# Kernel tuning notes

Measured on AMD Instinct MI355X. Metric: run time of the kernel, lower is better.

The kernel has to match this reference:

```python
import jax, jax.numpy as jnp
from jax import lax
import numpy as np

BN_EPS = 1e-5
LN_EPS = 1e-5


def _ln(x, g, b):
    m = x.mean(-1, keepdims=True)
    v = ((x - m) ** 2).mean(-1, keepdims=True)
    return (x - m) / jnp.sqrt(v + LN_EPS) * g + b


def _bn(x, g, b):
    # eval-mode BatchNorm2d with running_mean=0, running_var=1
    s = g / np.float32(np.sqrt(1.0 + BN_EPS))
    return x * s[None, :, None, None] + b[None, :, None, None]


def _conv(x, w, b, pad=0):
    y = lax.conv_general_dilated(x, w, (1, 1), [(pad, pad), (pad, pad)],
                                 dimension_numbers=('NCHW', 'OIHW', 'NCHW'))
    return y + b[None, :, None, None]


def _t2p(t, H, W):  # token2patch: [B,N,C] -> [B,C,H,W]
    B, N, C = t.shape
    return t.transpose(0, 2, 1).reshape(B, C, H, W)


def _p2t(x):  # patch2token: [B,C,H,W] -> [B,H*W,C]
    B, C, H, W = x.shape
    return x.reshape(B, C, H * W).transpose(0, 2, 1)


def _sgn(x, cw, cr_w, cr_b, ci_w, ci_b, g1, b1, g2, b2):
    # SpectralGatingNetwork. x: [B,C,H,W]; torch permute(0,3,2,1) -> [B,W,H,C]
    xp = x.transpose(0, 3, 2, 1)
    f = jnp.fft.rfft2(xp, axes=(1, 2), norm='ortho')  # [B,W,H//2+1,C]
    fr = jax.nn.relu(_bn(_conv(f.real.transpose(0, 3, 1, 2), cr_w, cr_b), g1, b1))
    fi = jax.nn.relu(_bn(_conv(f.imag.transpose(0, 3, 1, 2), ci_w, ci_b), g2, b2))
    fc = (fr + 1j * fi).transpose(0, 2, 3, 1) * (cw[..., 0] + 1j * cw[..., 1])
    out = jnp.fft.irfft2(fc, s=(xp.shape[1], xp.shape[2]), axes=(1, 2), norm='ortho')
    return out.transpose(0, 3, 2, 1)


def _forward(p):
    x = p['x']
    B, N, D = x.shape
    # ---- Attention_Module (self.sum) ----
    y = jax.nn.relu(x @ p['am_lin_w'] + p['am_lin_b'])  # [B,N,8]
    H, dh = 8, 1  # Attention(8, num_heads=8) -> head_dim 1, scale 1
    qkv = (y @ p['am_qkv_w'] + p['am_qkv_b']).reshape(B, N, 3, H, dh).transpose(2, 0, 3, 1, 4)
    q, k, v = qkv[0], qkv[1], qkv[2]
    attn = jax.nn.softmax(jnp.einsum('bhnd,bhmd->bhnm', q, k) * (dh ** -0.5), axis=-1)
    av = jnp.einsum('bhnm,bhmd->bhnd', attn, v).transpose(0, 2, 1, 3).reshape(B, N, 8)
    av = av @ p['am_proj_w'] + p['am_proj_b']
    x0 = _ln(x + (y + av) @ p['am_end_w'] + p['am_end_b'], p['am_ln_g'], p['am_ln_b'])
    # ---- mlp2(norm2(x0)), timm Mlp hidden=dim, exact GELU ----
    h = _ln(x0, p['ln2_g'], p['ln2_b'])
    x0 = jax.nn.gelu(h @ p['mlp_fc1_w'] + p['mlp_fc1_b'], approximate=False) @ p['mlp_fc2_w'] + p['mlp_fc2_b']
    # ---- adapter branch ----
    xa = x @ p['ad_w'] + p['ad_b']  # [B,320,8]
    z = _t2p(xa[:, :64], 8, 8)      # template tokens -> 8x8
    xr = _t2p(xa[:, 64:], 16, 16)   # search tokens -> 16x16
    # search-region branch
    x1 = jax.nn.relu(_bn(_conv(xr, p['b1_w'], p['b1_b']), p['b1_bn_g'], p['b1_bn_b']))
    xo = _sgn(x1, p['sx_cw'], p['sx_cr_w'], p['sx_cr_b'], p['sx_ci_w'], p['sx_ci_b'],
              p['sx_bn1_g'], p['sx_bn1_b'], p['sx_bn2_g'], p['sx_bn2_b']) + x1
    xo = _bn(_conv(xo, p['c1_w'], p['c1_b']), p['bn_g'], p['bn_b'])
    xo = jax.nn.relu(_p2t(xo))
    x2 = _conv(xr, p['c3_w'], p['c3_b'], pad=1)
    xo = _bn(_t2p(xo, 16, 16) + x2, p['bn_g'], p['bn_b'])
    xo = jax.nn.relu(_p2t(xo))
    # template branch
    z1 = jax.nn.relu(_bn(_conv(z, p['b2_w'], p['b2_b']), p['b2_bn_g'], p['b2_bn_b']))
    zo = _sgn(z1, p['sz_cw'], p['sz_cr_w'], p['sz_cr_b'], p['sz_ci_w'], p['sz_ci_b'],
              p['sz_bn1_g'], p['sz_bn1_b'], p['sz_bn2_g'], p['sz_bn2_b']) + z1
    zo = _bn(_conv(zo, p['c2_w'], p['c2_b']), p['bn_g'], p['bn_b'])
    zo = jax.nn.relu(_p2t(zo))
    z2 = _conv(z, p['c4_w'], p['c4_b'], pad=1)
    zo = _bn(_t2p(zo, 8, 8) + z2, p['bn_g'], p['bn_b'])
    zo = jax.nn.relu(_p2t(zo))
    xf = jnp.concatenate([zo, xo], axis=1) @ p['au_w'] + p['au_b']
    return xf + x0


def setup_inputs() -> dict:
    key = jax.random.key(0)
    ki = iter(jax.random.split(key, 64))
    def rn(shape, s=0.02):
        return jax.random.normal(next(ki), shape, dtype=jnp.float32) * s
    z8 = jnp.zeros((8,), jnp.float32)
    o8 = jnp.ones((8,), jnp.float32)
    z768 = jnp.zeros((768,), jnp.float32)
    o768 = jnp.ones((768,), jnp.float32)
    inp = dict(
        x=jax.random.normal(next(ki), (128, 320, 768), jnp.float32),
        am_lin_w=rn((768, 8)), am_lin_b=z8,
        am_qkv_w=rn((8, 24)), am_qkv_b=jnp.zeros((24,), jnp.float32),
        am_proj_w=rn((8, 8)), am_proj_b=z8,
        am_end_w=rn((8, 768)), am_end_b=z768,
        am_ln_g=o768, am_ln_b=z768,
        ln2_g=o768, ln2_b=z768,
        mlp_fc1_w=rn((768, 768)), mlp_fc1_b=z768,
        mlp_fc2_w=rn((768, 768)), mlp_fc2_b=z768,
        ad_w=rn((768, 8)), ad_b=z8,
        au_w=rn((8, 768)), au_b=z768,
        b1_w=rn((8, 8, 1, 1)), b1_b=z8, b1_bn_g=o8, b1_bn_b=z8,
        b2_w=rn((8, 8, 1, 1)), b2_b=z8, b2_bn_g=o8, b2_bn_b=z8,
        sx_cw=rn((16, 9, 8, 2)), sx_cr_w=rn((8, 8, 1, 1)), sx_cr_b=z8,
        sx_ci_w=rn((8, 8, 1, 1)), sx_ci_b=z8,
        sx_bn1_g=o8, sx_bn1_b=z8, sx_bn2_g=o8, sx_bn2_b=z8,
        sz_cw=rn((8, 5, 8, 2)), sz_cr_w=rn((8, 8, 1, 1)), sz_cr_b=z8,
        sz_ci_w=rn((8, 8, 1, 1)), sz_ci_b=z8,
        sz_bn1_g=o8, sz_bn1_b=z8, sz_bn2_g=o8, sz_bn2_b=z8,
        c1_w=rn((8, 8, 1, 1)), c1_b=z8, c2_w=rn((8, 8, 1, 1)), c2_b=z8,
        c3_w=rn((8, 8, 3, 3)), c3_b=z8, c4_w=rn((8, 8, 3, 3)), c4_b=z8,
        bn_g=o8, bn_b=z8,
    )
    return inp


def reference(x, am_lin_w, am_lin_b, am_qkv_w, am_qkv_b, am_proj_w, am_proj_b,
              am_end_w, am_end_b, am_ln_g, am_ln_b, ln2_g, ln2_b,
              mlp_fc1_w, mlp_fc1_b, mlp_fc2_w, mlp_fc2_b,
              ad_w, ad_b, au_w, au_b,
              b1_w, b1_b, b1_bn_g, b1_bn_b, b2_w, b2_b, b2_bn_g, b2_bn_b,
              sx_cw, sx_cr_w, sx_cr_b, sx_ci_w, sx_ci_b,
              sx_bn1_g, sx_bn1_b, sx_bn2_g, sx_bn2_b,
              sz_cw, sz_cr_w, sz_cr_b, sz_ci_w, sz_ci_b,
              sz_bn1_g, sz_bn1_b, sz_bn2_g, sz_bn2_b,
              c1_w, c1_b, c2_w, c2_b, c3_w, c3_b, c4_w, c4_b, bn_g, bn_b):
    return _forward(dict(locals()))
```

## Files before the change

kernel.cpp:

```cpp
#include <hip/hip_runtime.h>
#include <hip/hip_bf16.h>

typedef unsigned short u16;
typedef __bf16 bf16x8 __attribute__((ext_vector_type(8)));
typedef float f32x4 __attribute__((ext_vector_type(4)));

#define B_    128
#define N_TOK 320
#define D_    768
#define M_TOT (B_ * N_TOK)

__device__ __forceinline__ u16 f2b(float x) {
  __hip_bfloat16 t = __float2bfloat16(x);
  return *reinterpret_cast<u16*>(&t);
}

typedef const __attribute__((address_space(1))) void* gas1_t;
typedef __attribute__((address_space(3))) void* las3_t;
__device__ __forceinline__ void gll16(const void* g, void* l) {
  __builtin_amdgcn_global_load_lds((gas1_t)g, (las3_t)l, 16, 0, 0);
}

__device__ __forceinline__ void block_reduce2(float& a, float& b, float* red, int t) {
  #pragma unroll
  for (int off = 32; off >= 1; off >>= 1) {
    a += __shfl_xor(a, off);
    b += __shfl_xor(b, off);
  }
  int wv = t >> 6;
  __syncthreads();
  if ((t & 63) == 0) { red[wv] = a; red[4 + wv] = b; }
  __syncthreads();
  a = red[0] + red[1] + red[2] + red[3];
  b = red[4] + red[5] + red[6] + red[7];
}

__global__ __launch_bounds__(256) void k_transpose_bf16(const float* __restrict__ in,
                                                        u16* __restrict__ out) {
  __shared__ float tile[32][33];
  int c0 = blockIdx.x * 32, r0 = blockIdx.y * 32;
  int tx = threadIdx.x, ty = threadIdx.y;
  #pragma unroll
  for (int k = 0; k < 4; k++)
    tile[ty + k * 8][tx] = in[(size_t)(r0 + ty + k * 8) * 768 + c0 + tx];
  __syncthreads();
  #pragma unroll
  for (int k = 0; k < 4; k++)
    out[(size_t)(c0 + ty + k * 8) * 768 + r0 + tx] = f2b(tile[tx][ty + k * 8]);
}

__global__ __launch_bounds__(256) void k_token_a(
    const float* __restrict__ x,
    const float* __restrict__ lin_w, const float* __restrict__ lin_b,
    const float* __restrict__ qkv_w, const float* __restrict__ qkv_b,
    const float* __restrict__ ad_w, const float* __restrict__ ad_b,
    float* __restrict__ y_out, float* __restrict__ xa_out,
    float* __restrict__ q_out, float* __restrict__ k_out, float* __restrict__ v_out) {
  __shared__ __align__(16) float w_lds[16 * 768];
  int t = threadIdx.x;
  for (int i = t; i < 6144; i += 256) {
    w_lds[(i & 7) * 768 + (i >> 3)] = lin_w[i];
    w_lds[((i & 7) + 8) * 768 + (i >> 3)] = ad_w[i];
  }
  __syncthreads();
  int wave = t >> 6, lane = t & 63;
  for (int it = 0; it < 10; ++it) {
    int tok = blockIdx.x * 4 + wave + it * 4096;
    const float* xr = x + (size_t)tok * 768;
    float p[16];
    #pragma unroll
    for (int j = 0; j < 16; j++) p[j] = 0.f;
    #pragma unroll
    for (int u = 0; u < 3; u++) {
      float4 xv = *reinterpret_cast<const float4*>(xr + u * 256 + lane * 4);
      #pragma unroll
      for (int j = 0; j < 16; j++) {
        float4 wv = *reinterpret_cast<const float4*>(&w_lds[j * 768 + u * 256 + lane * 4]);
        p[j] += xv.x * wv.x + xv.y * wv.y + xv.z * wv.z + xv.w * wv.w;
      }
    }
    #pragma unroll
    for (int j = 0; j < 16; j++) {
      #pragma unroll
      for (int off = 32; off >= 1; off >>= 1) p[j] += __shfl_xor(p[j], off);
    }
    float yv[8];
    #pragma unroll
    for (int j = 0; j < 8; j++) yv[j] = fmaxf(p[j] + lin_b[j], 0.f);
    if (lane == 0) {
      #pragma unroll
      for (int j = 0; j < 8; j++) {
        y_out[(size_t)tok * 8 + j] = yv[j];
        xa_out[(size_t)tok * 8 + j] = p[8 + j] + ad_b[j];
      }
    }
    if (lane < 24) {
      float o = qkv_b[lane];
      #pragma unroll
      for (int j = 0; j < 8; j++) o += yv[j] * qkv_w[j * 24 + lane];
      int b = tok / 320, n = tok % 320;
      int hh = lane & 7;
      size_t idx = ((size_t)b * 8 + hh) * 320 + n;
      if (lane < 8) q_out[idx] = o;
      else if (lane < 16) k_out[idx] = o;
      else v_out[idx] = o;
    }
  }
}

__global__ __launch_bounds__(320) void k_attn(
    const float* __restrict__ q, const float* __restrict__ k,
    const float* __restrict__ v, float* __restrict__ av) {
  __shared__ float ks[320], vs[320];
  __shared__ float red[12];
  int bh = blockIdx.x;
  int n = threadIdx.x;
  float kk = k[(size_t)bh * 320 + n];
  ks[n] = kk;
  vs[n] = v[(size_t)bh * 320 + n];
  float qn = q[(size_t)bh * 320 + n];
  float mx = kk, mn = kk;
  #pragma unroll
  for (int off = 32; off >= 1; off >>= 1) {
    mx = fmaxf(mx, __shfl_xor(mx, off));
    mn = fminf(mn, __shfl_xor(mn, off));
  }
  int wave = n >> 6;
  if ((n & 63) == 0) { red[wave] = mx; red[5 + wave] = mn; }
  __syncthreads();
  if (n == 0) {
    float a = red[0], b = red[5];
    #pragma unroll
    for (int w = 1; w < 5; w++) { a = fmaxf(a, red[w]); b = fminf(b, red[5 + w]); }
    red[10] = a; red[11] = b;
  }
  __syncthreads();
  float kmax = red[10], kmin = red[11];
  float m1 = fmaxf(qn * kmax, qn * kmin);
  float se = 0.f, sv = 0.f;
  for (int m = 0; m < 320; m++) {
    float e = __expf(qn * ks[m] - m1);
    se += e;
    sv += e * vs[m];
  }
  int b_ = bh >> 3, h_ = bh & 7;
  av[(((size_t)b_ * 320) + n) * 8 + h_] = sv / se;
}

__global__ __launch_bounds__(256) void k_token_c(
    const float* __restrict__ x, const float* __restrict__ y_ws, const float* __restrict__ av_ws,
    const float* __restrict__ proj_w, const float* __restrict__ proj_b,
    const float* __restrict__ end_w, const float* __restrict__ end_b,
    const float* __restrict__ g1ln, const float* __restrict__ b1ln,
    const float* __restrict__ g2ln, const float* __restrict__ b2ln,
    u16* __restrict__ hout) {
  __shared__ float red[8];
  size_t tok = blockIdx.x;
  int t = threadIdx.x;
  float u[8];
  #pragma unroll
  for (int o = 0; o < 8; o++) {
    float a = proj_b[o];
    #pragma unroll
    for (int j = 0; j < 8; j++) a += av_ws[tok * 8 + j] * proj_w[j * 8 + o];
    u[o] = a + y_ws[tok * 8 + o];
  }
  float tv[3];
  #pragma unroll
  for (int c = 0; c < 3; c++) {
    int d = t + c * 256;
    float a = x[tok * 768 + d] + end_b[d];
    #pragma unroll
    for (int j = 0; j < 8; j++) a += u[j] * end_w[j * 768 + d];
    tv[c] = a;
  }
  float s = tv[0] + tv[1] + tv[2];
  float s2 = tv[0] * tv[0] + tv[1] * tv[1] + tv[2] * tv[2];
  block_reduce2(s, s2, red, t);
  float m1 = s * (1.f / 768.f);
  float inv1 = rsqrtf(fmaxf(s2 * (1.f / 768.f) - m1 * m1, 0.f) + 1e-5f);
  float x0[3];
  #pragma unroll
  for (int c = 0; c < 3; c++) {
    int d = t + c * 256;
    x0[c] = (tv[c] - m1) * inv1 * g1ln[d] + b1ln[d];
  }
  s = x0[0] + x0[1] + x0[2];
  s2 = x0[0] * x0[0] + x0[1] * x0[1] + x0[2] * x0[2];
  block_reduce2(s, s2, red, t);
  float m2 = s * (1.f / 768.f);
  float inv2 = rsqrtf(fmaxf(s2 * (1.f / 768.f) - m2 * m2, 0.f) + 1e-5f);
  #pragma unroll
  for (int c = 0; c < 3; c++) {
    int d = t + c * 256;
    float hv = (x0[c] - m2) * inv2 * g2ln[d] + b2ln[d];
    hout[tok * 768 + d] = f2b(hv);
  }
}

template <int S>
__global__ __launch_bounds__(256) void k_adapter(
    const float* __restrict__ xa,
    const float* __restrict__ bw, const float* __restrict__ bb,
    const float* __restrict__ bng0, const float* __restrict__ bnb0,
    const float* __restrict__ cw,
    const float* __restrict__ crw, const float* __restrict__ crb,
    const float* __restrict__ ciw, const float* __restrict__ cib,
    const float* __restrict__ bn1g, const float* __restrict__ bn1b,
    const float* __restrict__ bn2g, const float* __restrict__ bn2b,
    const float* __restrict__ cvw, const float* __restrict__ cvb,
    const float* __restrict__ c3w, const float* __restrict__ c3b,
    const float* __restrict__ bng, const float* __restrict__ bnb,
    float* __restrict__ crout, int tok_off) {
  constexpr int NF = S / 2 + 1;
  constexpr int P = S * S;
  constexpr int NFREQ = S * NF * 8;
  __shared__ float xr[8 * P];
  __shared__ float x1[8 * P];
  __shared__ float xo[8 * P];
  __shared__ float bufA[NFREQ * 2];
  __shared__ float bufB[NFREQ * 2];
  __shared__ float cosT[S], sinT[S];
  const int b = blockIdx.x, t = threadIdx.x;
  const float binv = rsqrtf(1.f + 1e-5f);
  if (t < S) {
    float ang = 6.28318530717958647692f * (float)t / (float)S;
    cosT[t] = cosf(ang);
    sinT[t] = sinf(ang);
  }
  for (int i = t; i < 8 * P; i += 256) {
    int c = i / P, p = i % P;
    xr[i] = xa[((size_t)b * N_TOK + tok_off + p) * 8 + c];
  }
  __syncthreads();
  for (int i = t; i < 8 * P; i += 256) {
    int c = i / P, p = i % P;
    float a = bb[c];
    #pragma unroll
    for (int j = 0; j < 8; j++) a += xr[j * P + p] * bw[c * 8 + j];
    a = a * (bng0[c] * binv) + bnb0[c];
    x1[i] = fmaxf(a, 0.f);
  }
  __syncthreads();
  for (int i = t; i < NFREQ; i += 256) {
    int c = i & 7, v = (i >> 3) % NF, w = i / (8 * NF);
    float re = 0.f, im = 0.f;
    #pragma unroll
    for (int h = 0; h < S; h++) {
      float xv = x1[c * P + h * S + w];
      int idx = (v * h) % S;
      re += xv * cosT[idx];
      im -= xv * sinT[idx];
    }
    bufA[i * 2] = re;
    bufA[i * 2 + 1] = im;
  }
  __syncthreads();
  for (int i = t; i < NFREQ; i += 256) {
    int c = i & 7, v = (i >> 3) % NF, u = i / (8 * NF);
    float re = 0.f, im = 0.f;
    #pragma unroll
    for (int w = 0; w < S; w++) {
      float ar = bufA[((w * NF + v) * 8 + c) * 2];
      float ai = bufA[((w * NF + v) * 8 + c) * 2 + 1];
      int idx = (u * w) % S;
      float cs = cosT[idx], sn = sinT[idx];
      re += ar * cs + ai * sn;
      im += ai * cs - ar * sn;
    }
    bufB[i * 2] = re * (1.f / S);
    bufB[i * 2 + 1] = im * (1.f / S);
  }
  __syncthreads();
  for (int i = t; i < NFREQ; i += 256) {
    int c = i & 7;
    int uv = i >> 3;
    float fr = crb[c], fi = cib[c];
    #pragma unroll
    for (int j = 0; j < 8; j++) {
      fr += bufB[(uv * 8 + j) * 2] * crw[c * 8 + j];
      fi += bufB[(uv * 8 + j) * 2 + 1] * ciw[c * 8 + j];
    }
    fr = fmaxf(fr * (bn1g[c] * binv) + bn1b[c], 0.f);
    fi = fmaxf(fi * (bn2g[c] * binv) + bn2b[c], 0.f);
    float cwr = cw[i * 2], cwi = cw[i * 2 + 1];
    bufA[i * 2] = fr * cwr - fi * cwi;
    bufA[i * 2 + 1] = fr * cwi + fi * cwr;
  }
  __syncthreads();
  for (int i = t; i < NFREQ; i += 256) {
    int c = i & 7, v = (i >> 3) % NF, w = i / (8 * NF);
    float re = 0.f, im = 0.f;
    #pragma unroll
    for (int u = 0; u < S; u++) {
      float gr = bufA[((u * NF + v) * 8 + c) * 2];
      float gi = bufA[((u * NF + v) * 8 + c) * 2 + 1];
      int idx = (u * w) % S;
      float cs = cosT[idx], sn = sinT[idx];
      re += gr * cs - gi * sn;
      im += gi * cs + gr * sn;
    }
    bufB[((w * NF + v) * 8 + c) * 2] = re;
    bufB[((w * NF + v) * 8 + c) * 2 + 1] = im;
  }
  __syncthreads();
  for (int i = t; i < 8 * P; i += 256) {
    int c = i / P, p = i % P, h = p / S, w = p % S;
    float acc = bufB[((w * NF + 0) * 8 + c) * 2];
    float ny = bufB[((w * NF + (NF - 1)) * 8 + c) * 2];
    acc += (h & 1) ? -ny : ny;
    #pragma unroll
    for (int v = 1; v < NF - 1; v++) {
      int idx = (v * h) % S;
      acc += 2.f * (bufB[((w * NF + v) * 8 + c) * 2] * cosT[idx] -
                    bufB[((w * NF + v) * 8 + c) * 2 + 1] * sinT[idx]);
    }
    xo[i] = acc * (1.f / S) + x1[i];
  }
  __syncthreads();
  for (int i = t; i < 8 * P; i += 256) {
    int c = i / P, p = i % P, h = p / S, w = p % S;
    float a = cvb[c];
    #pragma unroll
    for (int j = 0; j < 8; j++) a += xo[j * P + p] * cvw[c * 8 + j];
    a = fmaxf(a * (bng[c] * binv) + bnb[c], 0.f);
    float x2 = c3b[c];
    #pragma unroll
    for (int j = 0; j < 8; j++) {
      #pragma unroll
      for (int dy = 0; dy < 3; dy++) {
        int hh = h + dy - 1;
        if (hh < 0 || hh >= S) continue;
        #pragma unroll
        for (int dx = 0; dx < 3; dx++) {
          int ww = w + dx - 1;
          if (ww < 0 || ww >= S) continue;
          x2 += xr[j * P + hh * S + ww] * c3w[((c * 8 + j) * 3 + dy) * 3 + dx];
        }
      }
    }
    float fin = (a + x2) * (bng[c] * binv) + bnb[c];
    crout[((size_t)b * N_TOK + tok_off + p) * 8 + c] = fmaxf(fin, 0.f);
  }
}

template <int MODE>
__global__ __launch_bounds__(256, 2) void k_gemm(
    const u16* __restrict__ A, const u16* __restrict__ Bt,
    const float* __restrict__ bias,
    u16* __restrict__ obf, float* __restrict__ ofp,
    const float* __restrict__ au_w, const float* __restrict__ au_b,
    const float* __restrict__ cr) {
  __shared__ __align__(16) u16 As[2][128 * 64];
  __shared__ __align__(16) u16 Bs[2][128 * 64];
  int orig = blockIdx.x;
  int wgid = (orig & 7) * 240 + (orig >> 3);
  int bm = wgid / 6, bn = wgid % 6;
  int m0 = bm * 128, n0 = bn * 128;
  int t = threadIdx.x, wave = t >> 6, lane = t & 63;
  int wr = wave >> 1, wc = wave & 1;
  const int l15 = lane & 15, l4 = lane >> 4;
  const int swz = (l15 & 7) << 4;

  const char* srcA[4];
  const char* srcB[4];
  #pragma unroll
  for (int i = 0; i < 4; i++) {
    int b = i * 256 + t;
    int row = b >> 3;
    int colb = ((b & 7) << 4) ^ ((row & 7) << 4);
    srcA[i] = (const char*)A + (size_t)(m0 + row) * 1536 + colb;
    srcB[i] = (const char*)Bt + (size_t)(n0 + row) * 1536 + colb;
  }

  f32x4 acc[4][4];
  #pragma unroll
  for (int mi = 0; mi < 4; mi++)
    #pragma unroll
    for (int ni = 0; ni < 4; ni++) {
      f32x4 z = {0.f, 0.f, 0.f, 0.f};
      acc[mi][ni] = z;
    }

  auto STAGE = [&](int buf, int k0) {
    #pragma unroll
    for (int i = 0; i < 4; i++) {
      int basechunk = i * 256 + wave * 64;
      gll16(srcA[i] + 2 * k0, (void*)&As[buf][basechunk * 8]);
      gll16(srcB[i] + 2 * k0, (void*)&Bs[buf][basechunk * 8]);
    }
  };

  auto COMPUTE = [&](int buf) {
    const char* abase = (const char*)&As[buf][0];
    const char* bbase = (const char*)&Bs[buf][0];
    bf16x8 af[2][4], bf[2][4];
    #pragma unroll
    for (int kk = 0; kk < 2; kk++) {
      int c = kk * 64 + l4 * 16;
      int cs = c ^ swz;
      #pragma unroll
      for (int mi = 0; mi < 4; mi++) {
        int R = wr * 64 + mi * 16 + l15;
        af[kk][mi] = *reinterpret_cast<const bf16x8*>(abase + R * 128 + cs);
      }
      #pragma unroll
      for (int ni = 0; ni < 4; ni++) {
        int R = wc * 64 + ni * 16 + l15;
        bf[kk][ni] = *reinterpret_cast<const bf16x8*>(bbase + R * 128 + cs);
      }
    }
    #pragma unroll
    for (int kk = 0; kk < 2; kk++)
      #pragma unroll
      for (int mi = 0; mi < 4; mi++)
        #pragma unroll
        for (int ni = 0; ni < 4; ni++)
          acc[mi][ni] = __builtin_amdgcn_mfma_f32_16x16x32_bf16(af[kk][mi], bf[kk][ni],
                                                                acc[mi][ni], 0, 0, 0);
  };

  STAGE(0, 0);
  __syncthreads();
  int cur = 0;
  #pragma unroll 1
  for (int s = 0; s < 11; ++s) {
    STAGE(cur ^ 1, (s + 1) * 64);
    COMPUTE(cur);
    __syncthreads();
    cur ^= 1;
  }
  COMPUTE(cur);

  #pragma unroll
  for (int mi = 0; mi < 4; mi++) {
    #pragma unroll
    for (int ni = 0; ni < 4; ni++) {
      int colg = n0 + wc * 64 + ni * 16 + l15;
      #pragma unroll
      for (int rg = 0; rg < 4; rg++) {
        int rowg = m0 + wr * 64 + mi * 16 + l4 * 4 + rg;
        float vv = acc[mi][ni][rg] + bias[colg];
        if constexpr (MODE == 1) {
          vv = 0.5f * vv * (1.f + erff(vv * 0.70710678118654752f));
          obf[(size_t)rowg * 768 + colg] = f2b(vv);
        } else {
          vv += au_b[colg];
          const float* crr = cr + (size_t)rowg * 8;
          #pragma unroll
          for (int j = 0; j < 8; j++) vv += crr[j] * au_w[j * 768 + colg];
          ofp[(size_t)rowg * 768 + colg] = vv;
        }
      }
    }
  }
}

extern "C" void kernel_launch(void* const* d_in, const int* in_sizes, int n_in,
                              void* d_out, int out_size, void* d_ws, size_t ws_size,
                              hipStream_t stream) {
  const float* x        = (const float*)d_in[0];
  const float* am_lin_w = (const float*)d_in[1];
  const float* am_lin_b = (const float*)d_in[2];
  const float* am_qkv_w = (const float*)d_in[3];
  const float* am_qkv_b = (const float*)d_in[4];
  const float* am_proj_w= (const float*)d_in[5];
  const float* am_proj_b= (const float*)d_in[6];
  const float* am_end_w = (const float*)d_in[7];
  const float* am_end_b = (const float*)d_in[8];
  const float* am_ln_g  = (const float*)d_in[9];
  const float* am_ln_b  = (const float*)d_in[10];
  const float* ln2_g    = (const float*)d_in[11];
  const float* ln2_b    = (const float*)d_in[12];
  const float* fc1_w    = (const float*)d_in[13];
  const float* fc1_b    = (const float*)d_in[14];
  const float* fc2_w    = (const float*)d_in[15];
  const float* fc2_b    = (const float*)d_in[16];
  const float* ad_w     = (const float*)d_in[17];
  const float* ad_b     = (const float*)d_in[18];
  const float* au_w     = (const float*)d_in[19];
  const float* au_b     = (const float*)d_in[20];
  const float* b1_w     = (const float*)d_in[21];
  const float* b1_b     = (const float*)d_in[22];
  const float* b1_bn_g  = (const float*)d_in[23];
  const float* b1_bn_b  = (const float*)d_in[24];
  const float* b2_w     = (const float*)d_in[25];
  const float* b2_b     = (const float*)d_in[26];
  const float* b2_bn_g  = (const float*)d_in[27];
  const float* b2_bn_b  = (const float*)d_in[28];
  const float* sx_cw    = (const float*)d_in[29];
  const float* sx_cr_w  = (const float*)d_in[30];
  const float* sx_cr_b  = (const float*)d_in[31];
  const float* sx_ci_w  = (const float*)d_in[32];
  const float* sx_ci_b  = (const float*)d_in[33];
  const float* sx_bn1_g = (const float*)d_in[34];
  const float* sx_bn1_b = (const float*)d_in[35];
  const float* sx_bn2_g = (const float*)d_in[36];
  const float* sx_bn2_b = (const float*)d_in[37];
  const float* sz_cw    = (const float*)d_in[38];
  const float* sz_cr_w  = (const float*)d_in[39];
  const float* sz_cr_b  = (const float*)d_in[40];
  const float* sz_ci_w  = (const float*)d_in[41];
  const float* sz_ci_b  = (const float*)d_in[42];
  const float* sz_bn1_g = (const float*)d_in[43];
  const float* sz_bn1_b = (const float*)d_in[44];
  const float* sz_bn2_g = (const float*)d_in[45];
  const float* sz_bn2_b = (const float*)d_in[46];
  const float* c1_w     = (const float*)d_in[47];
  const float* c1_b     = (const float*)d_in[48];
  const float* c2_w     = (const float*)d_in[49];
  const float* c2_b     = (const float*)d_in[50];
  const float* c3_w     = (const float*)d_in[51];
  const float* c3_b     = (const float*)d_in[52];
  const float* c4_w     = (const float*)d_in[53];
  const float* c4_b     = (const float*)d_in[54];
  const float* bn_g     = (const float*)d_in[55];
  const float* bn_b     = (const float*)d_in[56];

  char* ws = (char*)d_ws;
  constexpr size_t H_OFF   = 0;
  constexpr size_t G1_OFF  = 62914560;
  constexpr size_t W1T_OFF = 125829120;
  constexpr size_t W2T_OFF = W1T_OFF + 1179648;
  constexpr size_t Y_OFF   = W2T_OFF + 1179648;
  constexpr size_t XA_OFF  = Y_OFF + 1310720;
  constexpr size_t AV_OFF  = XA_OFF + 1310720;
  constexpr size_t Q_OFF   = AV_OFF + 1310720;
  constexpr size_t K_OFF   = Q_OFF + 1310720;
  constexpr size_t V_OFF   = K_OFF + 1310720;
  constexpr size_t CR_OFF  = V_OFF + 1310720;

  u16* h_ws   = (u16*)(ws + H_OFF);
  u16* g1_ws  = (u16*)(ws + G1_OFF);
  u16* w1t    = (u16*)(ws + W1T_OFF);
  u16* w2t    = (u16*)(ws + W2T_OFF);
  float* y_ws = (float*)(ws + Y_OFF);
  float* xa_ws= (float*)(ws + XA_OFF);
  float* av_ws= (float*)(ws + AV_OFF);
  float* q_ws = (float*)(ws + Q_OFF);
  float* k_ws = (float*)(ws + K_OFF);
  float* v_ws = (float*)(ws + V_OFF);
  float* cr_ws= (float*)(ws + CR_OFF);

  k_transpose_bf16<<<dim3(24, 24), dim3(32, 8), 0, stream>>>(fc1_w, w1t);
  k_transpose_bf16<<<dim3(24, 24), dim3(32, 8), 0, stream>>>(fc2_w, w2t);
  k_token_a<<<1024, 256, 0, stream>>>(x, am_lin_w, am_lin_b, am_qkv_w, am_qkv_b,
                                      ad_w, ad_b, y_ws, xa_ws, q_ws, k_ws, v_ws);
  k_attn<<<1024, 320, 0, stream>>>(q_ws, k_ws, v_ws, av_ws);
  k_token_c<<<M_TOT, 256, 0, stream>>>(x, y_ws, av_ws, am_proj_w, am_proj_b,
                                       am_end_w, am_end_b, am_ln_g, am_ln_b,
                                       ln2_g, ln2_b, h_ws);
  k_adapter<8><<<128, 256, 0, stream>>>(xa_ws, b2_w, b2_b, b2_bn_g, b2_bn_b, sz_cw,
                                        sz_cr_w, sz_cr_b, sz_ci_w, sz_ci_b,
                                        sz_bn1_g, sz_bn1_b, sz_bn2_g, sz_bn2_b,
                                        c2_w, c2_b, c4_w, c4_b, bn_g, bn_b, cr_ws, 0);
  k_adapter<16><<<128, 256, 0, stream>>>(xa_ws, b1_w, b1_b, b1_bn_g, b1_bn_b, sx_cw,
                                         sx_cr_w, sx_cr_b, sx_ci_w, sx_ci_b,
                                         sx_bn1_g, sx_bn1_b, sx_bn2_g, sx_bn2_b,
                                         c1_w, c1_b, c3_w, c3_b, bn_g, bn_b, cr_ws, 64);
  k_gemm<1><<<1920, 256, 0, stream>>>(h_ws, w1t, fc1_b, g1_ws, nullptr, nullptr, nullptr, nullptr);
  k_gemm<2><<<1920, 256, 0, stream>>>(g1_ws, w2t, fc2_b, nullptr, (float*)d_out, au_w, au_b, cr_ws);
}
```

Baseline: 716.6 us.

## Use MFMA for token projections, fuse qkv into attention, deepen GEMM pipeline

Replaces the per-wave dot-product token kernel with a bf16 MFMA kernel that writes a combined y/xa buffer. The qkv projection moves into the attention kernel, and the separate q/k/v buffers are dropped. k_token_c switches to float4-vectorised loads and stores. The main GEMMs go from a 2-stage to a 4-stage LDS pipeline with explicit vmcnt waits and raw barriers, which drops occupancy to one block per CU. Rounding x to bf16 in the linear projections may slightly change accuracy.

```diff
diff --git a/kernel.cpp b/kernel.cpp
--- a/kernel.cpp
+++ b/kernel.cpp
@@ -20,6 +20,8 @@
 __device__ __forceinline__ void gll16(const void* g, void* l) {
   __builtin_amdgcn_global_load_lds((gas1_t)g, (las3_t)l, 16, 0, 0);
 }
+
+#define RAW_BARRIER() asm volatile("s_barrier" ::: "memory")
 
 __device__ __forceinline__ void block_reduce2(float& a, float& b, float* red, int t) {
   #pragma unroll
@@ -49,76 +51,73 @@
     out[(size_t)(c0 + ty + k * 8) * 768 + r0 + tx] = f2b(tile[tx][ty + k * 8]);
 }
 
-__global__ __launch_bounds__(256) void k_token_a(
+__global__ __launch_bounds__(256) void k_lin(
     const float* __restrict__ x,
     const float* __restrict__ lin_w, const float* __restrict__ lin_b,
-    const float* __restrict__ qkv_w, const float* __restrict__ qkv_b,
     const float* __restrict__ ad_w, const float* __restrict__ ad_b,
-    float* __restrict__ y_out, float* __restrict__ xa_out,
-    float* __restrict__ q_out, float* __restrict__ k_out, float* __restrict__ v_out) {
-  __shared__ __align__(16) float w_lds[16 * 768];
+    float* __restrict__ yxa) {
+  __shared__ __align__(16) u16 Wt[16 * 776];
   int t = threadIdx.x;
-  for (int i = t; i < 6144; i += 256) {
-    w_lds[(i & 7) * 768 + (i >> 3)] = lin_w[i];
-    w_lds[((i & 7) + 8) * 768 + (i >> 3)] = ad_w[i];
-  }
-  __syncthreads();
-  int wave = t >> 6, lane = t & 63;
-  for (int it = 0; it < 10; ++it) {
-    int tok = blockIdx.x * 4 + wave + it * 4096;
-    const float* xr = x + (size_t)tok * 768;
-    float p[16];
-    #pragma unroll
-    for (int j = 0; j < 16; j++) p[j] = 0.f;
-    #pragma unroll
-    for (int u = 0; u < 3; u++) {
-      float4 xv = *reinterpret_cast<const float4*>(xr + u * 256 + lane * 4);
-      #pragma unroll
-      for (int j = 0; j < 16; j++) {
-        float4 wv = *reinterpret_cast<const float4*>(&w_lds[j * 768 + u * 256 + lane * 4]);
-        p[j] += xv.x * wv.x + xv.y * wv.y + xv.z * wv.z + xv.w * wv.w;
-      }
-    }
-    #pragma unroll
-    for (int j = 0; j < 16; j++) {
-      #pragma unroll
-      for (int off = 32; off >= 1; off >>= 1) p[j] += __shfl_xor(p[j], off);
-    }
-    float yv[8];
-    #pragma unroll
-    for (int j = 0; j < 8; j++) yv[j] = fmaxf(p[j] + lin_b[j], 0.f);
-    if (lane == 0) {
-      #pragma unroll
-      for (int j = 0; j < 8; j++) {
-        y_out[(size_t)tok * 8 + j] = yv[j];
-        xa_out[(size_t)tok * 8 + j] = p[8 + j] + ad_b[j];
-      }
-    }
-    if (lane < 24) {
-      float o = qkv_b[lane];
-      #pragma unroll
-      for (int j = 0; j < 8; j++) o += yv[j] * qkv_w[j * 24 + lane];
-      int b = tok / 320, n = tok % 320;
-      int hh = lane & 7;
-      size_t idx = ((size_t)b * 8 + hh) * 320 + n;
-      if (lane < 8) q_out[idx] = o;
-      else if (lane < 16) k_out[idx] = o;
-      else v_out[idx] = o;
-    }
+  #pragma unroll 4
+  for (int r = 0; r < 48; r++) {
+    int i = r * 256 + t;
+    int j = i / 768, k = i - j * 768;
+    float w = (j < 8) ? lin_w[k * 8 + j] : ad_w[k * 8 + (j - 8)];
+    Wt[j * 776 + k] = f2b(w);
+  }
+  __syncthreads();
+  int wave = t >> 6, lane = t & 63, l15 = lane & 15, l4 = lane >> 4;
+  int m0 = blockIdx.x * 64 + wave * 16;
+  const float* xrow = x + (size_t)(m0 + l15) * 768 + l4 * 8;
+  f32x4 acc = {0.f, 0.f, 0.f, 0.f};
+  union BF8 { bf16x8 v; u16 s[8]; };
+  float4 c0 = *reinterpret_cast<const float4*>(xrow);
+  float4 c1 = *reinterpret_cast<const float4*>(xrow + 4);
+  #pragma unroll
+  for (int k = 0; k < 24; k++) {
+    float4 n0, n1;
+    if (k < 23) {
+      n0 = *reinterpret_cast<const float4*>(xrow + (k + 1) * 32);
+      n1 = *reinterpret_cast<const float4*>(xrow + (k + 1) * 32 + 4);
+    }
+    BF8 af;
+    af.s[0] = f2b(c0.x); af.s[1] = f2b(c0.y); af.s[2] = f2b(c0.z); af.s[3] = f2b(c0.w);
+    af.s[4] = f2b(c1.x); af.s[5] = f2b(c1.y); af.s[6] = f2b(c1.z); af.s[7] = f2b(c1.w);
+    bf16x8 wfrag = *reinterpret_cast<const bf16x8*>(&Wt[l15 * 776 + k * 32 + l4 * 8]);
+    acc = __builtin_amdgcn_mfma_f32_16x16x32_bf16(af.v, wfrag, acc, 0, 0, 0);
+    c0 = n0; c1 = n1;
+  }
+  int j = l15;
+  float bias = (j < 8) ? lin_b[j] : ad_b[j - 8];
+  #pragma unroll
+  for (int rg = 0; rg < 4; rg++) {
+    int tok = m0 + l4 * 4 + rg;
+    float v = acc[rg] + bias;
+    if (j < 8) v = fmaxf(v, 0.f);
+    yxa[(size_t)tok * 16 + j] = v;
   }
 }
 
 __global__ __launch_bounds__(320) void k_attn(
-    const float* __restrict__ q, const float* __restrict__ k,
-    const float* __restrict__ v, float* __restrict__ av) {
+    const float* __restrict__ yxa, const float* __restrict__ qkv_w,
+    const float* __restrict__ qkv_b, float* __restrict__ av) {
   __shared__ float ks[320], vs[320];
   __shared__ float red[12];
-  int bh = blockIdx.x;
+  int bh = blockIdx.x, b_ = bh >> 3, h_ = bh & 7;
   int n = threadIdx.x;
-  float kk = k[(size_t)bh * 320 + n];
+  const float* yr = yxa + ((size_t)b_ * 320 + n) * 16;
+  float4 y0 = *reinterpret_cast<const float4*>(yr);
+  float4 y1 = *reinterpret_cast<const float4*>(yr + 4);
+  float yv[8] = {y0.x, y0.y, y0.z, y0.w, y1.x, y1.y, y1.z, y1.w};
+  float qn = qkv_b[h_], kk = qkv_b[8 + h_], vv = qkv_b[16 + h_];
+  #pragma unroll
+  for (int j = 0; j < 8; j++) {
+    qn += yv[j] * qkv_w[j * 24 + h_];
+    kk += yv[j] * qkv_w[j * 24 + 8 + h_];
+    vv += yv[j] * qkv_w[j * 24 + 16 + h_];
+  }
   ks[n] = kk;
-  vs[n] = v[(size_t)bh * 320 + n];
-  float qn = q[(size_t)bh * 320 + n];
+  vs[n] = vv;
   float mx = kk, mn = kk;
   #pragma unroll
   for (int off = 32; off >= 1; off >>= 1) {
@@ -143,12 +142,11 @@
     se += e;
     sv += e * vs[m];
   }
-  int b_ = bh >> 3, h_ = bh & 7;
   av[(((size_t)b_ * 320) + n) * 8 + h_] = sv / se;
 }
 
 __global__ __launch_bounds__(256) void k_token_c(
-    const float* __restrict__ x, const float* __restrict__ y_ws, const float* __restrict__ av_ws,
+    const float* __restrict__ x, const float* __restrict__ yxa, const float* __restrict__ av_ws,
     const float* __restrict__ proj_w, const float* __restrict__ proj_b,
     const float* __restrict__ end_w, const float* __restrict__ end_b,
     const float* __restrict__ g1ln, const float* __restrict__ b1ln,
@@ -163,44 +161,57 @@
     float a = proj_b[o];
     #pragma unroll
     for (int j = 0; j < 8; j++) a += av_ws[tok * 8 + j] * proj_w[j * 8 + o];
-    u[o] = a + y_ws[tok * 8 + o];
-  }
-  float tv[3];
-  #pragma unroll
-  for (int c = 0; c < 3; c++) {
-    int d = t + c * 256;
-    float a = x[tok * 768 + d] + end_b[d];
-    #pragma unroll
-    for (int j = 0; j < 8; j++) a += u[j] * end_w[j * 768 + d];
-    tv[c] = a;
-  }
-  float s = tv[0] + tv[1] + tv[2];
-  float s2 = tv[0] * tv[0] + tv[1] * tv[1] + tv[2] * tv[2];
+    u[o] = a + yxa[tok * 16 + o];
+  }
+  const bool act = t < 192;
+  const int d0 = t * 4;
+  float tv[4] = {0.f, 0.f, 0.f, 0.f};
+  if (act) {
+    float4 xv = *reinterpret_cast<const float4*>(x + tok * 768 + d0);
+    float4 bv = *reinterpret_cast<const float4*>(end_b + d0);
+    tv[0] = xv.x + bv.x; tv[1] = xv.y + bv.y; tv[2] = xv.z + bv.z; tv[3] = xv.w + bv.w;
+    #pragma unroll
+    for (int j = 0; j < 8; j++) {
+      float4 wv = *reinterpret_cast<const float4*>(end_w + j * 768 + d0);
+      tv[0] += u[j] * wv.x; tv[1] += u[j] * wv.y;
+      tv[2] += u[j] * wv.z; tv[3] += u[j] * wv.w;
+    }
+  }
+  float s = tv[0] + tv[1] + tv[2] + tv[3];
+  float s2 = tv[0] * tv[0] + tv[1] * tv[1] + tv[2] * tv[2] + tv[3] * tv[3];
   block_reduce2(s, s2, red, t);
   float m1 = s * (1.f / 768.f);
   float inv1 = rsqrtf(fmaxf(s2 * (1.f / 768.f) - m1 * m1, 0.f) + 1e-5f);
-  float x0[3];
-  #pragma unroll
-  for (int c = 0; c < 3; c++) {
-    int d = t + c * 256;
-    x0[c] = (tv[c] - m1) * inv1 * g1ln[d] + b1ln[d];
-  }
-  s = x0[0] + x0[1] + x0[2];
-  s2 = x0[0] * x0[0] + x0[1] * x0[1] + x0[2] * x0[2];
-  block_reduce2(s, s2, red, t);
-  float m2 = s * (1.f / 768.f);
-  float inv2 = rsqrtf(fmaxf(s2 * (1.f / 768.f) - m2 * m2, 0.f) + 1e-5f);
-  #pragma unroll
-  for (int c = 0; c < 3; c++) {
-    int d = t + c * 256;
-    float hv = (x0[c] - m2) * inv2 * g2ln[d] + b2ln[d];
-    hout[tok * 768 + d] = f2b(hv);
+  float x0[4];
+  float sb = 0.f, sb2 = 0.f;
+  if (act) {
+    float4 g1 = *reinterpret_cast<const float4*>(g1ln + d0);
+    float4 bb1 = *reinterpret_cast<const float4*>(b1ln + d0);
+    x0[0] = (tv[0] - m1) * inv1 * g1.x + bb1.x;
+    x0[1] = (tv[1] - m1) * inv1 * g1.y + bb1.y;
+    x0[2] = (tv[2] - m1) * inv1 * g1.z + bb1.z;
+    x0[3] = (tv[3] - m1) * inv1 * g1.w + bb1.w;
+    sb = x0[0] + x0[1] + x0[2] + x0[3];
+    sb2 = x0[0] * x0[0] + x0[1] * x0[1] + x0[2] * x0[2] + x0[3] * x0[3];
+  }
+  block_reduce2(sb, sb2, red, t);
+  float m2 = sb * (1.f / 768.f);
+  float inv2 = rsqrtf(fmaxf(sb2 * (1.f / 768.f) - m2 * m2, 0.f) + 1e-5f);
+  if (act) {
+    float4 g2 = *reinterpret_cast<const float4*>(g2ln + d0);
+    float4 bb2 = *reinterpret_cast<const float4*>(b2ln + d0);
+    short4 hv;
+    hv.x = (short)f2b((x0[0] - m2) * inv2 * g2.x + bb2.x);
+    hv.y = (short)f2b((x0[1] - m2) * inv2 * g2.y + bb2.y);
+    hv.z = (short)f2b((x0[2] - m2) * inv2 * g2.z + bb2.z);
+    hv.w = (short)f2b((x0[3] - m2) * inv2 * g2.w + bb2.w);
+    *reinterpret_cast<short4*>(hout + tok * 768 + d0) = hv;
   }
 }
 
 template <int S>
 __global__ __launch_bounds__(256) void k_adapter(
-    const float* __restrict__ xa,
+    const float* __restrict__ yxa,
     const float* __restrict__ bw, const float* __restrict__ bb,
     const float* __restrict__ bng0, const float* __restrict__ bnb0,
     const float* __restrict__ cw,
@@ -230,7 +241,7 @@
   }
   for (int i = t; i < 8 * P; i += 256) {
     int c = i / P, p = i % P;
-    xr[i] = xa[((size_t)b * N_TOK + tok_off + p) * 8 + c];
+    xr[i] = yxa[((size_t)b * N_TOK + tok_off + p) * 16 + 8 + c];
   }
   __syncthreads();
   for (int i = t; i < 8 * P; i += 256) {
@@ -345,14 +356,14 @@
 }
 
 template <int MODE>
-__global__ __launch_bounds__(256, 2) void k_gemm(
+__global__ __launch_bounds__(256, 1) void k_gemm(
     const u16* __restrict__ A, const u16* __restrict__ Bt,
     const float* __restrict__ bias,
     u16* __restrict__ obf, float* __restrict__ ofp,
     const float* __restrict__ au_w, const float* __restrict__ au_b,
     const float* __restrict__ cr) {
-  __shared__ __align__(16) u16 As[2][128 * 64];
-  __shared__ __align__(16) u16 Bs[2][128 * 64];
+  __shared__ __align__(16) u16 As[4][128 * 64];
+  __shared__ __align__(16) u16 Bs[4][128 * 64];
   int orig = blockIdx.x;
   int wgid = (orig & 7) * 240 + (orig >> 3);
   int bm = wgid / 6, bn = wgid % 6;
@@ -382,12 +393,12 @@
       acc[mi][ni] = z;
     }
 
-  auto STAGE = [&](int buf, int k0) {
+  auto STAGE = [&](int buf, int tile) {
     #pragma unroll
     for (int i = 0; i < 4; i++) {
       int basechunk = i * 256 + wave * 64;
-      gll16(srcA[i] + 2 * k0, (void*)&As[buf][basechunk * 8]);
-      gll16(srcB[i] + 2 * k0, (void*)&Bs[buf][basechunk * 8]);
+      gll16(srcA[i] + 128 * tile, (void*)&As[buf][basechunk * 8]);
+      gll16(srcB[i] + 128 * tile, (void*)&Bs[buf][basechunk * 8]);
     }
   };
 
@@ -397,8 +408,7 @@
     bf16x8 af[2][4], bf[2][4];
     #pragma unroll
     for (int kk = 0; kk < 2; kk++) {
-      int c = kk * 64 + l4 * 16;
-      int cs = c ^ swz;
+      int cs = (kk * 64 + l4 * 16) ^ swz;
       #pragma unroll
       for (int mi = 0; mi < 4; mi++) {
         int R = wr * 64 + mi * 16 + l15;
@@ -420,17 +430,22 @@
                                                                 acc[mi][ni], 0, 0, 0);
   };
 
-  STAGE(0, 0);
-  __syncthreads();
-  int cur = 0;
-  #pragma unroll 1
-  for (int s = 0; s < 11; ++s) {
-    STAGE(cur ^ 1, (s + 1) * 64);
-    COMPUTE(cur);
-    __syncthreads();
-    cur ^= 1;
-  }
-  COMPUTE(cur);
+  STAGE(0, 0); STAGE(1, 1); STAGE(2, 2); STAGE(3, 3);
+  #pragma unroll
+  for (int s = 0; s < 12; ++s) {
+    if (s < 9)        asm volatile("s_waitcnt vmcnt(24)" ::: "memory");
+    else if (s == 9)  asm volatile("s_waitcnt vmcnt(16)" ::: "memory");
+    else if (s == 10) asm volatile("s_waitcnt vmcnt(8)" ::: "memory");
+    else              asm volatile("s_waitcnt vmcnt(0)" ::: "memory");
+    RAW_BARRIER();
+    __builtin_amdgcn_sched_barrier(0);
+    COMPUTE(s & 3);
+    if (s < 8) {
+      RAW_BARRIER();
+      __builtin_amdgcn_sched_barrier(0);
+      STAGE(s & 3, s + 4);
+    }
+  }
 
   #pragma unroll
   for (int mi = 0; mi < 4; mi++) {
@@ -522,39 +537,30 @@
   constexpr size_t G1_OFF  = 62914560;
   constexpr size_t W1T_OFF = 125829120;
   constexpr size_t W2T_OFF = W1T_OFF + 1179648;
-  constexpr size_t Y_OFF   = W2T_OFF + 1179648;
-  constexpr size_t XA_OFF  = Y_OFF + 1310720;
-  constexpr size_t AV_OFF  = XA_OFF + 1310720;
-  constexpr size_t Q_OFF   = AV_OFF + 1310720;
-  constexpr size_t K_OFF   = Q_OFF + 1310720;
-  constexpr size_t V_OFF   = K_OFF + 1310720;
-  constexpr size_t CR_OFF  = V_OFF + 1310720;
-
-  u16* h_ws   = (u16*)(ws + H_OFF);
-  u16* g1_ws  = (u16*)(ws + G1_OFF);
-  u16* w1t    = (u16*)(ws + W1T_OFF);
-  u16* w2t    = (u16*)(ws + W2T_OFF);
-  float* y_ws = (float*)(ws + Y_OFF);
-  float* xa_ws= (float*)(ws + XA_OFF);
-  float* av_ws= (float*)(ws + AV_OFF);
-  float* q_ws = (float*)(ws + Q_OFF);
-  float* k_ws = (float*)(ws + K_OFF);
-  float* v_ws = (float*)(ws + V_OFF);
-  float* cr_ws= (float*)(ws + CR_OFF);
+  constexpr size_t YXA_OFF = W2T_OFF + 1179648;
+  constexpr size_t AV_OFF  = YXA_OFF + 2621440;
+  constexpr size_t CR_OFF  = AV_OFF + 1310720;
+
+  u16* h_ws    = (u16*)(ws + H_OFF);
+  u16* g1_ws   = (u16*)(ws + G1_OFF);
+  u16* w1t     = (u16*)(ws + W1T_OFF);
+  u16* w2t     = (u16*)(ws + W2T_OFF);
+  float* yxa_ws= (float*)(ws + YXA_OFF);
+  float* av_ws = (float*)(ws + AV_OFF);
+  float* cr_ws = (float*)(ws + CR_OFF);
 
   k_transpose_bf16<<<dim3(24, 24), dim3(32, 8), 0, stream>>>(fc1_w, w1t);
   k_transpose_bf16<<<dim3(24, 24), dim3(32, 8), 0, stream>>>(fc2_w, w2t);
-  k_token_a<<<1024, 256, 0, stream>>>(x, am_lin_w, am_lin_b, am_qkv_w, am_qkv_b,
-                                      ad_w, ad_b, y_ws, xa_ws, q_ws, k_ws, v_ws);
-  k_attn<<<1024, 320, 0, stream>>>(q_ws, k_ws, v_ws, av_ws);
-  k_token_c<<<M_TOT, 256, 0, stream>>>(x, y_ws, av_ws, am_proj_w, am_proj_b,
+  k_lin<<<640, 256, 0, stream>>>(x, am_lin_w, am_lin_b, ad_w, ad_b, yxa_ws);
+  k_attn<<<1024, 320, 0, stream>>>(yxa_ws, am_qkv_w, am_qkv_b, av_ws);
+  k_token_c<<<M_TOT, 256, 0, stream>>>(x, yxa_ws, av_ws, am_proj_w, am_proj_b,
                                        am_end_w, am_end_b, am_ln_g, am_ln_b,
                                        ln2_g, ln2_b, h_ws);
-  k_adapter<8><<<128, 256, 0, stream>>>(xa_ws, b2_w, b2_b, b2_bn_g, b2_bn_b, sz_cw,
+  k_adapter<8><<<128, 256, 0, stream>>>(yxa_ws, b2_w, b2_b, b2_bn_g, b2_bn_b, sz_cw,
                                         sz_cr_w, sz_cr_b, sz_ci_w, sz_ci_b,
                                         sz_bn1_g, sz_bn1_b, sz_bn2_g, sz_bn2_b,
                                         c2_w, c2_b, c4_w, c4_b, bn_g, bn_b, cr_ws, 0);
-  k_adapter<16><<<128, 256, 0, stream>>>(xa_ws, b1_w, b1_b, b1_bn_g, b1_bn_b, sx_cw,
+  k_adapter<16><<<128, 256, 0, stream>>>(yxa_ws, b1_w, b1_b, b1_bn_g, b1_bn_b, sx_cw,
                                          sx_cr_w, sx_cr_b, sx_ci_w, sx_ci_b,
                                          sx_bn1_g, sx_bn1_b, sx_bn2_g, sx_bn2_b,
                                          c1_w, c1_b, c3_w, c3_b, bn_g, bn_b, cr_ws, 64);
```

After: 804.5 us. +12.3%, slower.
